# Kernel tuning notes

Measured on AMD Instinct MI355X. Metric: run time of the kernel, lower is better.

## Reference

```python
import jax, jax.numpy as jnp
import numpy as np

N = 50000        # number of nodes
E = 1600000      # number of (directed) edges, ~degree 32
D = 128          # latent_dim
L = 2            # num_layers
NEG_SLOPE = 0.01 # torch F.leaky_relu default


def setup_inputs() -> dict:
    key = jax.random.key(0)
    k1, k2, k3, k4 = jax.random.split(key, 4)
    h = jax.random.normal(k1, (N, D), dtype=jnp.float32)
    src = jax.random.randint(k2, (E,), 0, N, dtype=jnp.int32)
    dst = jax.random.randint(k3, (E,), 0, N, dtype=jnp.int32)
    # attn_fc per layer: Linear(2*D, 1, bias=False) -> weight vector of length 2*D
    att_w = jax.random.normal(k4, (L, 2 * D), dtype=jnp.float32) * 0.1
    return {"h": h, "src": src, "dst": dst, "att_w": att_w}


def _segment_softmax(e, seg, n):
    # numerically-stable softmax over edges grouped by destination node
    m = jax.ops.segment_max(e, seg, num_segments=n)      # [N]
    ex = jnp.exp(e - m[seg])                             # [E]
    s = jax.ops.segment_sum(ex, seg, num_segments=n)     # [N]
    return ex / s[seg]


def reference(h, src, dst, att_w):
    n, d = h.shape
    for l in range(att_w.shape[0]):
        w_src = att_w[l, :d]   # weight applied to edges.src['h']
        w_dst = att_w[l, d:]   # weight applied to edges.dst['h']
        # a = attn_fc(concat(h_src, h_dst)) = h_src @ w_src + h_dst @ w_dst
        a = h[src] @ w_src + h[dst] @ w_dst               # [E]
        e = jnp.where(a > 0, a, NEG_SLOPE * a)            # leaky_relu
        alpha = _segment_softmax(e, dst, n)               # edge_softmax by dst
        # update_all: m = h_src * e ; h_dst = sum(m)
        h = jax.ops.segment_sum(h[src] * alpha[:, None], dst, num_segments=n)
    return h
```

## Files before the change

### kernel.cpp

```cpp
#include <hip/hip_runtime.h>
#include <hip/hip_fp16.h>
#include <math.h>

#define NEG_SLOPE 0.01f
#define BKT_BITS 7
#define BKT_MASK 127
#define SBLOCKS  256
#define STPB     512


__global__ void build_st_kernel(const int* __restrict__ dst, int* __restrict__ blockhist,
                                int E, int NB, int nq, int qchunk,
                                const float* __restrict__ h, const float* __restrict__ att_w_l,
                                float* __restrict__ s, float* __restrict__ t,
                                __half* __restrict__ h16, int N) {
    extern __shared__ int lh[];
    if (blockIdx.x < SBLOCKS) {
        for (int k = threadIdx.x; k < NB; k += blockDim.x) lh[k] = 0;
        __syncthreads();
        int b = blockIdx.x;
        int qbeg = b * qchunk, qend = min(nq, qbeg + qchunk);
        for (int q = qbeg + (int)threadIdx.x; q < qend; q += blockDim.x) {
            int e = q << 2;
            if (e + 3 < E) {
                int4 d4 = *(const int4*)(dst + e);
                atomicAdd(&lh[d4.x >> BKT_BITS], 1);
                atomicAdd(&lh[d4.y >> BKT_BITS], 1);
                atomicAdd(&lh[d4.z >> BKT_BITS], 1);
                atomicAdd(&lh[d4.w >> BKT_BITS], 1);
            } else {
                for (int j = e; j < E; ++j) atomicAdd(&lh[dst[j] >> BKT_BITS], 1);
            }
        }
        __syncthreads();
        for (int k = threadIdx.x; k < NB; k += blockDim.x)
            blockhist[k * SBLOCKS + blockIdx.x] = lh[k];
    } else {
        int sb  = blockIdx.x - SBLOCKS;
        int gid = sb * (int)blockDim.x + threadIdx.x;
        int wid = gid >> 6;
        int lane = threadIdx.x & 63;
        int half = lane >> 5;
        int hl   = lane & 31;
        int v    = wid * 2 + half;
        if (v >= N) return;
        float4 hv = ((const float4*)(h + (size_t)v * 128))[hl];
        __half2 p01 = __floats2half2_rn(hv.x, hv.y);
        __half2 p23 = __floats2half2_rn(hv.z, hv.w);
        float2 packed;
        packed.x = *(const float*)&p01;
        packed.y = *(const float*)&p23;
        ((float2*)(h16 + (size_t)v * 128))[hl] = packed;
        float4 ws = ((const float4*)att_w_l)[hl];
        float4 wd = ((const float4*)(att_w_l + 128))[hl];
        float ps = hv.x * ws.x + hv.y * ws.y + hv.z * ws.z + hv.w * ws.w;
        float pt = hv.x * wd.x + hv.y * wd.y + hv.z * wd.z + hv.w * wd.w;
        for (int off = 16; off > 0; off >>= 1) {
            ps += __shfl_down(ps, off);
            pt += __shfl_down(pt, off);
        }
        if (hl == 0) { s[v] = ps; t[v] = pt; }
    }
}

__global__ void scan1_kernel(const int* __restrict__ in, int* __restrict__ local_excl,
                             int* __restrict__ partials, int n) {
    __shared__ int sm[1024];
    int i = blockIdx.x * 1024 + threadIdx.x;
    int x = (i < n) ? in[i] : 0;
    sm[threadIdx.x] = x;
    __syncthreads();
    for (int off = 1; off < 1024; off <<= 1) {
        int y = (threadIdx.x >= (unsigned)off) ? sm[threadIdx.x - off] : 0;
        __syncthreads();
        sm[threadIdx.x] += y;
        __syncthreads();
    }
    if (i < n) local_excl[i] = sm[threadIdx.x] - x;
    if (threadIdx.x == 1023) partials[blockIdx.x] = sm[1023];
}

__global__ void scan2_kernel(int* __restrict__ partials, int nchunks) {
    __shared__ int sm[1024];
    int x = (threadIdx.x < (unsigned)nchunks) ? partials[threadIdx.x] : 0;
    sm[threadIdx.x] = x;
    __syncthreads();
    for (int off = 1; off < 1024; off <<= 1) {
        int y = (threadIdx.x >= (unsigned)off) ? sm[threadIdx.x - off] : 0;
        __syncthreads();
        sm[threadIdx.x] += y;
        __syncthreads();
    }
    partials[threadIdx.x] = sm[threadIdx.x] - x;
    if (threadIdx.x == 1023) partials[1024] = sm[1023];
}

__device__ __forceinline__ int bh_at(const int* __restrict__ local_ex,
                                     const int* __restrict__ partials, int i) {
    return local_ex[i] + partials[i >> 10];
}

__global__ void bksplit_kernel(const int* __restrict__ src, const int* __restrict__ dst,
                               const int* __restrict__ local_ex, const int* __restrict__ partials,
                               unsigned* __restrict__ pairs,
                               int E, int NB, int nq, int qchunk) {
    extern __shared__ int lm[];
    int* lbase = lm;
    int* lcnt  = lm + NB;
    int b = blockIdx.x;
    for (int k = threadIdx.x; k < NB; k += blockDim.x) {
        lbase[k] = bh_at(local_ex, partials, k * SBLOCKS + b);
        lcnt[k]  = 0;
    }
    __syncthreads();
    int qbeg = b * qchunk, qend = min(nq, qbeg + qchunk);
    for (int q = qbeg + (int)threadIdx.x; q < qend; q += blockDim.x) {
        int e = q << 2;
        if (e + 3 < E) {
            int4 d4 = *(const int4*)(dst + e);
            int4 s4 = *(const int4*)(src + e);
            int k0 = d4.x >> BKT_BITS;
            int p0 = lbase[k0] + atomicAdd(&lcnt[k0], 1);
            pairs[p0] = ((unsigned)s4.x << BKT_BITS) | (unsigned)(d4.x & BKT_MASK);
            int k1 = d4.y >> BKT_BITS;
            int p1 = lbase[k1] + atomicAdd(&lcnt[k1], 1);
            pairs[p1] = ((unsigned)s4.y << BKT_BITS) | (unsigned)(d4.y & BKT_MASK);
            int k2 = d4.z >> BKT_BITS;
            int p2 = lbase[k2] + atomicAdd(&lcnt[k2], 1);
            pairs[p2] = ((unsigned)s4.z << BKT_BITS) | (unsigned)(d4.z & BKT_MASK);
            int k3 = d4.w >> BKT_BITS;
            int p3 = lbase[k3] + atomicAdd(&lcnt[k3], 1);
            pairs[p3] = ((unsigned)s4.w << BKT_BITS) | (unsigned)(d4.w & BKT_MASK);
        } else {
            for (int j = e; j < E; ++j) {
                int d = dst[j];
                int k = d >> BKT_BITS;
                int pos = lbase[k] + atomicAdd(&lcnt[k], 1);
                pairs[pos] = ((unsigned)src[j] << BKT_BITS) | (unsigned)(d & BKT_MASK);
            }
        }
    }
}

__global__ void csr_build_kernel(const unsigned* __restrict__ pairs,
                                 const int* __restrict__ local_ex, const int* __restrict__ partials,
                                 int* __restrict__ row_ptr, int* __restrict__ csr_src,
                                 int E, int N, int NB) {
    __shared__ int ldeg[128];
    __shared__ int lscan[128];
    __shared__ int lpos[128];
    int k = blockIdx.x;
    int bbase = bh_at(local_ex, partials, k * SBLOCKS);
    int bend  = (k == NB - 1) ? E : bh_at(local_ex, partials, (k + 1) * SBLOCKS);
    if (threadIdx.x < 128) ldeg[threadIdx.x] = 0;
    __syncthreads();
    for (int i = bbase + (int)threadIdx.x; i < bend; i += blockDim.x)
        atomicAdd(&ldeg[pairs[i] & BKT_MASK], 1);
    __syncthreads();
    int x = (threadIdx.x < 128) ? ldeg[threadIdx.x] : 0;
    if (threadIdx.x < 128) lscan[threadIdx.x] = x;
    __syncthreads();
    for (int off = 1; off < 128; off <<= 1) {
        int y = 0;
        if (threadIdx.x < 128 && threadIdx.x >= (unsigned)off) y = lscan[threadIdx.x - off];
        __syncthreads();
        if (threadIdx.x < 128) lscan[threadIdx.x] += y;
        __syncthreads();
    }
    if (threadIdx.x < 128) {
        int excl = lscan[threadIdx.x] - x;
        int node = (k << BKT_BITS) + threadIdx.x;
        if (node < N) row_ptr[node] = bbase + excl;
        lpos[threadIdx.x] = excl;
    }
    if (k == NB - 1 && threadIdx.x == 0) row_ptr[N] = E;
    __syncthreads();
    for (int i = bbase + (int)threadIdx.x; i < bend; i += blockDim.x) {
        unsigned p = pairs[i];
        int pos = atomicAdd(&lpos[p & BKT_MASK], 1);
        csr_src[bbase + pos] = (int)(p >> BKT_BITS);
    }
}


__device__ __forceinline__ void gath8(const __half* __restrict__ hin, int u, float w,
                                      int qlane, float acc[8]) {
    float4 r = ((const float4*)(hin + ((size_t)(unsigned)u << 7)))[qlane];
    const __half2* hp = (const __half2*)&r;
    #pragma unroll
    for (int d = 0; d < 4; ++d) {
        acc[2 * d]     = fmaf(__low2float(hp[d]),  w, acc[2 * d]);
        acc[2 * d + 1] = fmaf(__high2float(hp[d]), w, acc[2 * d + 1]);
    }
}

template<bool LAST>
__global__ __launch_bounds__(256, 8)
void agg_kernel(const __half* __restrict__ hin, const float* __restrict__ s,
                const float* __restrict__ t, const int* __restrict__ row_ptr,
                const int* __restrict__ csr_src,
                __half* __restrict__ hout16, float* __restrict__ outf,
                const float* __restrict__ att_w_next,
                float* __restrict__ s2, float* __restrict__ t2, int n) {
    int gid   = blockIdx.x * blockDim.x + threadIdx.x;
    int v     = gid >> 6;
    int lane  = threadIdx.x & 63;
    if (v >= n) return;
    int quad  = lane >> 4;
    int qlane = lane & 15;

    int beg = row_ptr[v];
    int end = row_ptr[v + 1];
    float tv = t[v];

    float acc[8] = {0.f, 0.f, 0.f, 0.f, 0.f, 0.f, 0.f, 0.f};
    float lsum_l = 0.f;

    for (int base = beg; base < end; base += 64) {
        int cnt = end - base;
        if (cnt > 64) cnt = 64;
        int idx = base + min(lane, cnt - 1);
        int u   = csr_src[idx];
        float a = s[u] + tv;
        float e = (a > 0.f) ? a : NEG_SLOPE * a;
        float wl = (lane < cnt) ? __expf(e) : 0.f;
        lsum_l += wl;
        int steps = (cnt + 3) >> 2;
        int k = 0;
        for (; k + 3 < steps; k += 4) {
            int sl0 = (k << 2) + quad;
            int   u0 = __shfl(u, sl0);       float w0 = __shfl(wl, sl0);
            int   u1 = __shfl(u, sl0 + 4);   float w1 = __shfl(wl, sl0 + 4);
            int   u2 = __shfl(u, sl0 + 8);   float w2 = __shfl(wl, sl0 + 8);
            int   u3 = __shfl(u, sl0 + 12);  float w3 = __shfl(wl, sl0 + 12);
            gath8(hin, u0, w0, qlane, acc);
            gath8(hin, u1, w1, qlane, acc);
            gath8(hin, u2, w2, qlane, acc);
            gath8(hin, u3, w3, qlane, acc);
        }
        for (; k < steps; ++k) {
            int sl = (k << 2) + quad;
            int   u0 = __shfl(u, sl);
            float w0 = __shfl(wl, sl);
            gath8(hin, u0, w0, qlane, acc);
        }
    }
    #pragma unroll
    for (int j = 0; j < 8; ++j) {
        acc[j] += __shfl_xor(acc[j], 16);
        acc[j] += __shfl_xor(acc[j], 32);
    }
    float lsum = lsum_l;
    for (int off = 32; off > 0; off >>= 1) lsum += __shfl_xor(lsum, off);
    float inv_l = (lsum > 0.f) ? (1.0f / lsum) : 0.f;
    #pragma unroll
    for (int j = 0; j < 8; ++j) acc[j] *= inv_l;

    if (LAST) {
        if (quad == 0) {
            float4* op = (float4*)(outf + (size_t)v * 128);
            op[2 * qlane]     = make_float4(acc[0], acc[1], acc[2], acc[3]);
            op[2 * qlane + 1] = make_float4(acc[4], acc[5], acc[6], acc[7]);
        }
    } else {
        if (quad == 0) {
            __half2 p0 = __floats2half2_rn(acc[0], acc[1]);
            __half2 p1 = __floats2half2_rn(acc[2], acc[3]);
            __half2 p2 = __floats2half2_rn(acc[4], acc[5]);
            __half2 p3 = __floats2half2_rn(acc[6], acc[7]);
            int4 pk;
            pk.x = *(const int*)&p0; pk.y = *(const int*)&p1;
            pk.z = *(const int*)&p2; pk.w = *(const int*)&p3;
            ((int4*)(hout16 + (size_t)v * 128))[qlane] = pk;
        }
        float4 ws0 = ((const float4*)att_w_next)[2 * qlane];
        float4 ws1 = ((const float4*)att_w_next)[2 * qlane + 1];
        float4 wd0 = ((const float4*)(att_w_next + 128))[2 * qlane];
        float4 wd1 = ((const float4*)(att_w_next + 128))[2 * qlane + 1];
        float ps = acc[0] * ws0.x + acc[1] * ws0.y + acc[2] * ws0.z + acc[3] * ws0.w
                 + acc[4] * ws1.x + acc[5] * ws1.y + acc[6] * ws1.z + acc[7] * ws1.w;
        float pt = acc[0] * wd0.x + acc[1] * wd0.y + acc[2] * wd0.z + acc[3] * wd0.w
                 + acc[4] * wd1.x + acc[5] * wd1.y + acc[6] * wd1.z + acc[7] * wd1.w;
        for (int off = 8; off > 0; off >>= 1) {
            ps += __shfl_down(ps, off);
            pt += __shfl_down(pt, off);
        }
        if (lane == 0) { s2[v] = ps; t2[v] = pt; }
    }
}


extern "C" void kernel_launch(void* const* d_in, const int* in_sizes, int n_in,
                              void* d_out, int out_size, void* d_ws, size_t ws_size,
                              hipStream_t stream) {
    const float* h0    = (const float*)d_in[0];
    const int*   src   = (const int*)d_in[1];
    const int*   dst   = (const int*)d_in[2];
    const float* att_w = (const float*)d_in[3];
    int N = in_sizes[0] / 128;
    int E = in_sizes[1];
    int L = in_sizes[3] / 256;
    float* out = (float*)d_out;

    int NB = (N + BKT_MASK) >> BKT_BITS;
    int n2 = NB * SBLOCKS;
    int nq = (E + 3) >> 2;
    int qchunk = (nq + SBLOCKS - 1) / SBLOCKS;
    int nch2 = (n2 + 1023) / 1024;

    char* ws = (char*)d_ws;
    size_t off = 0;
    auto alloc = [&](size_t bytes) -> void* {
        void* p = ws + off;
        off = (off + bytes + 511) & ~(size_t)511;
        return p;
    };
    int*      row_ptr   = (int*)     alloc((size_t)(N + 1) * 4);
    int*      csr_src   = (int*)     alloc((size_t)E * 4);
    float*    s1        = (float*)   alloc((size_t)N * 4);
    float*    t1        = (float*)   alloc((size_t)N * 4);
    float*    s2        = (float*)   alloc((size_t)N * 4);
    float*    t2        = (float*)   alloc((size_t)N * 4);
    __half*   hA        = (__half*)  alloc((size_t)N * 128 * 2);
    __half*   hB        = (__half*)  alloc((size_t)N * 128 * 2);
    unsigned* pairs     = (unsigned*)alloc((size_t)E * 4);
    int*      blockhist = (int*)     alloc((size_t)n2 * 4);
    int*      local_ex  = (int*)     alloc((size_t)n2 * 4);
    int*      partials  = (int*)     alloc(1025 * 4);

    int st_blocks = ((N + 1) / 2 + 7) / 8;
    build_st_kernel<<<SBLOCKS + st_blocks, STPB, NB * 4, stream>>>(
        dst, blockhist, E, NB, nq, qchunk, h0, att_w, s1, t1, hA, N);
    scan1_kernel<<<nch2, 1024, 0, stream>>>(blockhist, local_ex, partials, n2);
    scan2_kernel<<<1, 1024, 0, stream>>>(partials, nch2);
    bksplit_kernel<<<SBLOCKS, STPB, 2 * NB * 4, stream>>>(src, dst, local_ex, partials,
                                                          pairs, E, NB, nq, qchunk);
    csr_build_kernel<<<NB, 512, 0, stream>>>(pairs, local_ex, partials,
                                             row_ptr, csr_src, E, N, NB);

    const int tb = 256;
    int node_blocks = (N * 64 + tb - 1) / tb;

    __half* hin = hA;
    __half* hnx = hB;
    float *sc = s1, *tc = t1, *sn = s2, *tn = t2;
    for (int l = 0; l < L; ++l) {
        if (l == L - 1) {
            agg_kernel<true><<<node_blocks, tb, 0, stream>>>(
                hin, sc, tc, row_ptr, csr_src, nullptr, out, nullptr, nullptr, nullptr, N);
        } else {
            agg_kernel<false><<<node_blocks, tb, 0, stream>>>(
                hin, sc, tc, row_ptr, csr_src, hnx, nullptr,
                att_w + (size_t)(l + 1) * 256, sn, tn, N);
            __half* tmp = hin; hin = hnx; hnx = tmp;
            float* tf;
            tf = sc; sc = sn; sn = tf;
            tf = tc; tc = tn; tn = tf;
        }
    }
}
```

Before: 214.9 us.

## Fuse CSR build pipeline into one cooperative kernel with grid syncs

```diff
diff --git a/kernel.cpp b/kernel.cpp
--- a/kernel.cpp
+++ b/kernel.cpp
@@ -1,184 +1,161 @@
 #include <hip/hip_runtime.h>
 #include <hip/hip_fp16.h>
+#include <hip/hip_cooperative_groups.h>
 #include <math.h>
+
+namespace cg = cooperative_groups;
 
 #define NEG_SLOPE 0.01f
 #define BKT_BITS 7
 #define BKT_MASK 127
 #define SBLOCKS  256
 #define STPB     512
-
-
-__global__ void build_st_kernel(const int* __restrict__ dst, int* __restrict__ blockhist,
-                                int E, int NB, int nq, int qchunk,
-                                const float* __restrict__ h, const float* __restrict__ att_w_l,
-                                float* __restrict__ s, float* __restrict__ t,
-                                __half* __restrict__ h16, int N) {
-    extern __shared__ int lh[];
-    if (blockIdx.x < SBLOCKS) {
-        for (int k = threadIdx.x; k < NB; k += blockDim.x) lh[k] = 0;
-        __syncthreads();
-        int b = blockIdx.x;
-        int qbeg = b * qchunk, qend = min(nq, qbeg + qchunk);
-        for (int q = qbeg + (int)threadIdx.x; q < qend; q += blockDim.x) {
+#define MAXNB    512
+
+__global__ void build_coop_kernel(const int* __restrict__ src, const int* __restrict__ dst,
+                                  const float* __restrict__ h, const float* __restrict__ att_w_l,
+                                  int* __restrict__ g_total, unsigned* __restrict__ pairs,
+                                  int* __restrict__ row_ptr, int* __restrict__ csr_src,
+                                  float* __restrict__ s, float* __restrict__ t,
+                                  __half* __restrict__ h16,
+                                  int E, int N, int NB, int nq, int qchunk) {
+    __shared__ int lh[MAXNB];
+    __shared__ int lbb[MAXNB];
+    __shared__ int sc[STPB];
+    __shared__ int lstart[MAXNB + 1];
+    __shared__ int ldeg[128];
+    __shared__ int lscan[128];
+    __shared__ int lpos[128];
+
+    cg::grid_group grid = cg::this_grid();
+    int b   = blockIdx.x;
+    int tid = threadIdx.x;
+
+    for (int k = tid; k < NB; k += blockDim.x) lh[k] = 0;
+    __syncthreads();
+    int qbeg = b * qchunk, qend = min(nq, qbeg + qchunk);
+    for (int q = qbeg + tid; q < qend; q += blockDim.x) {
+        int e = q << 2;
+        if (e + 3 < E) {
+            int4 d4 = *(const int4*)(dst + e);
+            atomicAdd(&lh[d4.x >> BKT_BITS], 1);
+            atomicAdd(&lh[d4.y >> BKT_BITS], 1);
+            atomicAdd(&lh[d4.z >> BKT_BITS], 1);
+            atomicAdd(&lh[d4.w >> BKT_BITS], 1);
+        } else {
+            for (int j = e; j < E; ++j) atomicAdd(&lh[dst[j] >> BKT_BITS], 1);
+        }
+    }
+    __syncthreads();
+    for (int k = tid; k < NB; k += blockDim.x)
+        lbb[k] = atomicAdd(&g_total[k], lh[k]);
+
+    {
+        int lane = tid & 63;
+        int halfw = lane >> 5;
+        int hl = lane & 31;
+        int wv = b * (blockDim.x >> 6) + (tid >> 6);
+        int vstride = gridDim.x * (blockDim.x >> 6) * 2;
+        for (int v = wv * 2 + halfw; v < N; v += vstride) {
+            float4 hv = ((const float4*)(h + (size_t)v * 128))[hl];
+            __half2 p01 = __floats2half2_rn(hv.x, hv.y);
+            __half2 p23 = __floats2half2_rn(hv.z, hv.w);
+            float2 packed;
+            packed.x = *(const float*)&p01;
+            packed.y = *(const float*)&p23;
+            ((float2*)(h16 + (size_t)v * 128))[hl] = packed;
+            float4 ws = ((const float4*)att_w_l)[hl];
+            float4 wd = ((const float4*)(att_w_l + 128))[hl];
+            float ps = hv.x * ws.x + hv.y * ws.y + hv.z * ws.z + hv.w * ws.w;
+            float pt = hv.x * wd.x + hv.y * wd.y + hv.z * wd.z + hv.w * wd.w;
+            for (int off = 16; off > 0; off >>= 1) {
+                ps += __shfl_down(ps, off);
+                pt += __shfl_down(pt, off);
+            }
+            if (hl == 0) { s[v] = ps; t[v] = pt; }
+        }
+    }
+    grid.sync();
+
+    {
+        int x = (tid < NB) ? g_total[tid] : 0;
+        sc[tid] = x;
+        __syncthreads();
+        for (int off = 1; off < STPB; off <<= 1) {
+            int y = (tid >= (unsigned)off) ? sc[tid - off] : 0;
+            __syncthreads();
+            sc[tid] += y;
+            __syncthreads();
+        }
+        if (tid < NB) lstart[tid] = sc[tid] - x;
+        if (tid == 0) lstart[NB] = E;
+        __syncthreads();
+        for (int k = tid; k < NB; k += blockDim.x) {
+            lbb[k] += lstart[k];
+            lh[k] = 0;
+        }
+        __syncthreads();
+        for (int q = qbeg + tid; q < qend; q += blockDim.x) {
             int e = q << 2;
             if (e + 3 < E) {
                 int4 d4 = *(const int4*)(dst + e);
-                atomicAdd(&lh[d4.x >> BKT_BITS], 1);
-                atomicAdd(&lh[d4.y >> BKT_BITS], 1);
-                atomicAdd(&lh[d4.z >> BKT_BITS], 1);
-                atomicAdd(&lh[d4.w >> BKT_BITS], 1);
+                int4 s4 = *(const int4*)(src + e);
+                int k0 = d4.x >> BKT_BITS;
+                int p0 = lbb[k0] + atomicAdd(&lh[k0], 1);
+                pairs[p0] = ((unsigned)s4.x << BKT_BITS) | (unsigned)(d4.x & BKT_MASK);
+                int k1 = d4.y >> BKT_BITS;
+                int p1 = lbb[k1] + atomicAdd(&lh[k1], 1);
+                pairs[p1] = ((unsigned)s4.y << BKT_BITS) | (unsigned)(d4.y & BKT_MASK);
+                int k2 = d4.z >> BKT_BITS;
+                int p2 = lbb[k2] + atomicAdd(&lh[k2], 1);
+                pairs[p2] = ((unsigned)s4.z << BKT_BITS) | (unsigned)(d4.z & BKT_MASK);
+                int k3 = d4.w >> BKT_BITS;
+                int p3 = lbb[k3] + atomicAdd(&lh[k3], 1);
+                pairs[p3] = ((unsigned)s4.w << BKT_BITS) | (unsigned)(d4.w & BKT_MASK);
             } else {
-                for (int j = e; j < E; ++j) atomicAdd(&lh[dst[j] >> BKT_BITS], 1);
+                for (int j = e; j < E; ++j) {
+                    int d = dst[j];
+                    int k = d >> BKT_BITS;
+                    int pos = lbb[k] + atomicAdd(&lh[k], 1);
+                    pairs[pos] = ((unsigned)src[j] << BKT_BITS) | (unsigned)(d & BKT_MASK);
+                }
             }
         }
-        __syncthreads();
-        for (int k = threadIdx.x; k < NB; k += blockDim.x)
-            blockhist[k * SBLOCKS + blockIdx.x] = lh[k];
-    } else {
-        int sb  = blockIdx.x - SBLOCKS;
-        int gid = sb * (int)blockDim.x + threadIdx.x;
-        int wid = gid >> 6;
-        int lane = threadIdx.x & 63;
-        int half = lane >> 5;
-        int hl   = lane & 31;
-        int v    = wid * 2 + half;
-        if (v >= N) return;
-        float4 hv = ((const float4*)(h + (size_t)v * 128))[hl];
-        __half2 p01 = __floats2half2_rn(hv.x, hv.y);
-        __half2 p23 = __floats2half2_rn(hv.z, hv.w);
-        float2 packed;
-        packed.x = *(const float*)&p01;
-        packed.y = *(const float*)&p23;
-        ((float2*)(h16 + (size_t)v * 128))[hl] = packed;
-        float4 ws = ((const float4*)att_w_l)[hl];
-        float4 wd = ((const float4*)(att_w_l + 128))[hl];
-        float ps = hv.x * ws.x + hv.y * ws.y + hv.z * ws.z + hv.w * ws.w;
-        float pt = hv.x * wd.x + hv.y * wd.y + hv.z * wd.z + hv.w * wd.w;
-        for (int off = 16; off > 0; off >>= 1) {
-            ps += __shfl_down(ps, off);
-            pt += __shfl_down(pt, off);
-        }
-        if (hl == 0) { s[v] = ps; t[v] = pt; }
-    }
-}
-
-__global__ void scan1_kernel(const int* __restrict__ in, int* __restrict__ local_excl,
-                             int* __restrict__ partials, int n) {
-    __shared__ int sm[1024];
-    int i = blockIdx.x * 1024 + threadIdx.x;
-    int x = (i < n) ? in[i] : 0;
-    sm[threadIdx.x] = x;
-    __syncthreads();
-    for (int off = 1; off < 1024; off <<= 1) {
-        int y = (threadIdx.x >= (unsigned)off) ? sm[threadIdx.x - off] : 0;
-        __syncthreads();
-        sm[threadIdx.x] += y;
-        __syncthreads();
-    }
-    if (i < n) local_excl[i] = sm[threadIdx.x] - x;
-    if (threadIdx.x == 1023) partials[blockIdx.x] = sm[1023];
-}
-
-__global__ void scan2_kernel(int* __restrict__ partials, int nchunks) {
-    __shared__ int sm[1024];
-    int x = (threadIdx.x < (unsigned)nchunks) ? partials[threadIdx.x] : 0;
-    sm[threadIdx.x] = x;
-    __syncthreads();
-    for (int off = 1; off < 1024; off <<= 1) {
-        int y = (threadIdx.x >= (unsigned)off) ? sm[threadIdx.x - off] : 0;
-        __syncthreads();
-        sm[threadIdx.x] += y;
-        __syncthreads();
-    }
-    partials[threadIdx.x] = sm[threadIdx.x] - x;
-    if (threadIdx.x == 1023) partials[1024] = sm[1023];
-}
-
-__device__ __forceinline__ int bh_at(const int* __restrict__ local_ex,
-                                     const int* __restrict__ partials, int i) {
-    return local_ex[i] + partials[i >> 10];
-}
-
-__global__ void bksplit_kernel(const int* __restrict__ src, const int* __restrict__ dst,
-                               const int* __restrict__ local_ex, const int* __restrict__ partials,
-                               unsigned* __restrict__ pairs,
-                               int E, int NB, int nq, int qchunk) {
-    extern __shared__ int lm[];
-    int* lbase = lm;
-    int* lcnt  = lm + NB;
-    int b = blockIdx.x;
-    for (int k = threadIdx.x; k < NB; k += blockDim.x) {
-        lbase[k] = bh_at(local_ex, partials, k * SBLOCKS + b);
-        lcnt[k]  = 0;
-    }
-    __syncthreads();
-    int qbeg = b * qchunk, qend = min(nq, qbeg + qchunk);
-    for (int q = qbeg + (int)threadIdx.x; q < qend; q += blockDim.x) {
-        int e = q << 2;
-        if (e + 3 < E) {
-            int4 d4 = *(const int4*)(dst + e);
-            int4 s4 = *(const int4*)(src + e);
-            int k0 = d4.x >> BKT_BITS;
-            int p0 = lbase[k0] + atomicAdd(&lcnt[k0], 1);
-            pairs[p0] = ((unsigned)s4.x << BKT_BITS) | (unsigned)(d4.x & BKT_MASK);
-            int k1 = d4.y >> BKT_BITS;
-            int p1 = lbase[k1] + atomicAdd(&lcnt[k1], 1);
-            pairs[p1] = ((unsigned)s4.y << BKT_BITS) | (unsigned)(d4.y & BKT_MASK);
-            int k2 = d4.z >> BKT_BITS;
-            int p2 = lbase[k2] + atomicAdd(&lcnt[k2], 1);
-            pairs[p2] = ((unsigned)s4.z << BKT_BITS) | (unsigned)(d4.z & BKT_MASK);
-            int k3 = d4.w >> BKT_BITS;
-            int p3 = lbase[k3] + atomicAdd(&lcnt[k3], 1);
-            pairs[p3] = ((unsigned)s4.w << BKT_BITS) | (unsigned)(d4.w & BKT_MASK);
-        } else {
-            for (int j = e; j < E; ++j) {
-                int d = dst[j];
-                int k = d >> BKT_BITS;
-                int pos = lbase[k] + atomicAdd(&lcnt[k], 1);
-                pairs[pos] = ((unsigned)src[j] << BKT_BITS) | (unsigned)(d & BKT_MASK);
-            }
-        }
-    }
-}
-
-__global__ void csr_build_kernel(const unsigned* __restrict__ pairs,
-                                 const int* __restrict__ local_ex, const int* __restrict__ partials,
-                                 int* __restrict__ row_ptr, int* __restrict__ csr_src,
-                                 int E, int N, int NB) {
-    __shared__ int ldeg[128];
-    __shared__ int lscan[128];
-    __shared__ int lpos[128];
-    int k = blockIdx.x;
-    int bbase = bh_at(local_ex, partials, k * SBLOCKS);
-    int bend  = (k == NB - 1) ? E : bh_at(local_ex, partials, (k + 1) * SBLOCKS);
-    if (threadIdx.x < 128) ldeg[threadIdx.x] = 0;
-    __syncthreads();
-    for (int i = bbase + (int)threadIdx.x; i < bend; i += blockDim.x)
-        atomicAdd(&ldeg[pairs[i] & BKT_MASK], 1);
-    __syncthreads();
-    int x = (threadIdx.x < 128) ? ldeg[threadIdx.x] : 0;
-    if (threadIdx.x < 128) lscan[threadIdx.x] = x;
-    __syncthreads();
-    for (int off = 1; off < 128; off <<= 1) {
-        int y = 0;
-        if (threadIdx.x < 128 && threadIdx.x >= (unsigned)off) y = lscan[threadIdx.x - off];
-        __syncthreads();
-        if (threadIdx.x < 128) lscan[threadIdx.x] += y;
-        __syncthreads();
-    }
-    if (threadIdx.x < 128) {
-        int excl = lscan[threadIdx.x] - x;
-        int node = (k << BKT_BITS) + threadIdx.x;
-        if (node < N) row_ptr[node] = bbase + excl;
-        lpos[threadIdx.x] = excl;
-    }
-    if (k == NB - 1 && threadIdx.x == 0) row_ptr[N] = E;
-    __syncthreads();
-    for (int i = bbase + (int)threadIdx.x; i < bend; i += blockDim.x) {
-        unsigned p = pairs[i];
-        int pos = atomicAdd(&lpos[p & BKT_MASK], 1);
-        csr_src[bbase + pos] = (int)(p >> BKT_BITS);
+    }
+    grid.sync();
+
+    if (b == 0 && tid == 0) row_ptr[N] = E;
+    for (int kb = b; kb < NB; kb += gridDim.x) {
+        int bbase = lstart[kb];
+        int bend  = lstart[kb + 1];
+        if (tid < 128) ldeg[tid] = 0;
+        __syncthreads();
+        for (int i = bbase + tid; i < bend; i += blockDim.x)
+            atomicAdd(&ldeg[pairs[i] & BKT_MASK], 1);
+        __syncthreads();
+        int x = (tid < 128) ? ldeg[tid] : 0;
+        if (tid < 128) lscan[tid] = x;
+        __syncthreads();
+        for (int off = 1; off < 128; off <<= 1) {
+            int y = 0;
+            if (tid < 128 && tid >= (unsigned)off) y = lscan[tid - off];
+            __syncthreads();
+            if (tid < 128) lscan[tid] += y;
+            __syncthreads();
+        }
+        if (tid < 128) {
+            int excl = lscan[tid] - x;
+            int node = (kb << BKT_BITS) + tid;
+            if (node < N) row_ptr[node] = bbase + excl;
+            lpos[tid] = excl;
+        }
+        __syncthreads();
+        for (int i = bbase + tid; i < bend; i += blockDim.x) {
+            unsigned p = pairs[i];
+            int pos = atomicAdd(&lpos[p & BKT_MASK], 1);
+            csr_src[bbase + pos] = (int)(p >> BKT_BITS);
+        }
+        __syncthreads();
     }
 }
 
@@ -303,10 +280,8 @@
     float* out = (float*)d_out;
 
     int NB = (N + BKT_MASK) >> BKT_BITS;
-    int n2 = NB * SBLOCKS;
     int nq = (E + 3) >> 2;
     int qchunk = (nq + SBLOCKS - 1) / SBLOCKS;
-    int nch2 = (n2 + 1023) / 1024;
 
     char* ws = (char*)d_ws;
     size_t off = 0;
@@ -324,19 +299,18 @@
     __half*   hA        = (__half*)  alloc((size_t)N * 128 * 2);
     __half*   hB        = (__half*)  alloc((size_t)N * 128 * 2);
     unsigned* pairs     = (unsigned*)alloc((size_t)E * 4);
-    int*      blockhist = (int*)     alloc((size_t)n2 * 4);
-    int*      local_ex  = (int*)     alloc((size_t)n2 * 4);
-    int*      partials  = (int*)     alloc(1025 * 4);
-
-    int st_blocks = ((N + 1) / 2 + 7) / 8;
-    build_st_kernel<<<SBLOCKS + st_blocks, STPB, NB * 4, stream>>>(
-        dst, blockhist, E, NB, nq, qchunk, h0, att_w, s1, t1, hA, N);
-    scan1_kernel<<<nch2, 1024, 0, stream>>>(blockhist, local_ex, partials, n2);
-    scan2_kernel<<<1, 1024, 0, stream>>>(partials, nch2);
-    bksplit_kernel<<<SBLOCKS, STPB, 2 * NB * 4, stream>>>(src, dst, local_ex, partials,
-                                                          pairs, E, NB, nq, qchunk);
-    csr_build_kernel<<<NB, 512, 0, stream>>>(pairs, local_ex, partials,
-                                             row_ptr, csr_src, E, N, NB);
+    int*      g_total   = (int*)     alloc((size_t)(NB + 1) * 4);
+
+    hipMemsetAsync(g_total, 0, (size_t)NB * 4, stream);
+
+    void* cargs[] = {
+        (void*)&src, (void*)&dst, (void*)&h0, (void*)&att_w,
+        (void*)&g_total, (void*)&pairs, (void*)&row_ptr, (void*)&csr_src,
+        (void*)&s1, (void*)&t1, (void*)&hA,
+        (void*)&E, (void*)&N, (void*)&NB, (void*)&nq, (void*)&qchunk
+    };
+    hipLaunchCooperativeKernel(reinterpret_cast<void*>(build_coop_kernel),
+                               dim3(SBLOCKS), dim3(STPB), cargs, 0, stream);
 
     const int tb = 256;
     int node_blocks = (N * 64 + tb - 1) / tb;
```

Result: slower. 303.5 us (+41.2%).

## Replace two-pass global scan with atomic bucket offsets and per-block scan

Applied to the files above, without the earlier changes.

```diff
diff --git a/kernel.cpp b/kernel.cpp
--- a/kernel.cpp
+++ b/kernel.cpp
@@ -7,9 +7,11 @@
 #define BKT_MASK 127
 #define SBLOCKS  256
 #define STPB     512
-
-
-__global__ void build_st_kernel(const int* __restrict__ dst, int* __restrict__ blockhist,
+#define MAXNB    512
+
+
+__global__ void build_st_kernel(const int* __restrict__ dst, int* __restrict__ g_total,
+                                int* __restrict__ g_lbb,
                                 int E, int NB, int nq, int qchunk,
                                 const float* __restrict__ h, const float* __restrict__ att_w_l,
                                 float* __restrict__ s, float* __restrict__ t,
@@ -34,7 +36,7 @@
         }
         __syncthreads();
         for (int k = threadIdx.x; k < NB; k += blockDim.x)
-            blockhist[k * SBLOCKS + blockIdx.x] = lh[k];
+            g_lbb[k * SBLOCKS + b] = atomicAdd(&g_total[k], lh[k]);
     } else {
         int sb  = blockIdx.x - SBLOCKS;
         int gid = sb * (int)blockDim.x + threadIdx.x;
@@ -63,58 +65,40 @@
     }
 }
 
-__global__ void scan1_kernel(const int* __restrict__ in, int* __restrict__ local_excl,
-                             int* __restrict__ partials, int n) {
-    __shared__ int sm[1024];
-    int i = blockIdx.x * 1024 + threadIdx.x;
-    int x = (i < n) ? in[i] : 0;
-    sm[threadIdx.x] = x;
-    __syncthreads();
-    for (int off = 1; off < 1024; off <<= 1) {
-        int y = (threadIdx.x >= (unsigned)off) ? sm[threadIdx.x - off] : 0;
-        __syncthreads();
-        sm[threadIdx.x] += y;
-        __syncthreads();
-    }
-    if (i < n) local_excl[i] = sm[threadIdx.x] - x;
-    if (threadIdx.x == 1023) partials[blockIdx.x] = sm[1023];
-}
-
-__global__ void scan2_kernel(int* __restrict__ partials, int nchunks) {
-    __shared__ int sm[1024];
-    int x = (threadIdx.x < (unsigned)nchunks) ? partials[threadIdx.x] : 0;
-    sm[threadIdx.x] = x;
-    __syncthreads();
-    for (int off = 1; off < 1024; off <<= 1) {
-        int y = (threadIdx.x >= (unsigned)off) ? sm[threadIdx.x - off] : 0;
-        __syncthreads();
-        sm[threadIdx.x] += y;
-        __syncthreads();
-    }
-    partials[threadIdx.x] = sm[threadIdx.x] - x;
-    if (threadIdx.x == 1023) partials[1024] = sm[1023];
-}
-
-__device__ __forceinline__ int bh_at(const int* __restrict__ local_ex,
-                                     const int* __restrict__ partials, int i) {
-    return local_ex[i] + partials[i >> 10];
-}
-
 __global__ void bksplit_kernel(const int* __restrict__ src, const int* __restrict__ dst,
-                               const int* __restrict__ local_ex, const int* __restrict__ partials,
-                               unsigned* __restrict__ pairs,
+                               const int* __restrict__ g_total, const int* __restrict__ g_lbb,
+                               int* __restrict__ g_lstart, unsigned* __restrict__ pairs,
                                int E, int NB, int nq, int qchunk) {
-    extern __shared__ int lm[];
-    int* lbase = lm;
-    int* lcnt  = lm + NB;
-    int b = blockIdx.x;
-    for (int k = threadIdx.x; k < NB; k += blockDim.x) {
-        lbase[k] = bh_at(local_ex, partials, k * SBLOCKS + b);
+    __shared__ int sc[STPB];
+    __shared__ int lstart[MAXNB + 1];
+    __shared__ int lbase[MAXNB];
+    __shared__ int lcnt[MAXNB];
+    int b   = blockIdx.x;
+    int tid = threadIdx.x;
+
+    int x = (tid < NB) ? g_total[tid] : 0;
+    sc[tid] = x;
+    __syncthreads();
+    for (int off = 1; off < STPB; off <<= 1) {
+        int y = (tid >= (unsigned)off) ? sc[tid - off] : 0;
+        __syncthreads();
+        sc[tid] += y;
+        __syncthreads();
+    }
+    if (tid < NB) lstart[tid] = sc[tid] - x;
+    if (tid == 0) lstart[NB] = E;
+    __syncthreads();
+    for (int k = tid; k < NB; k += blockDim.x) {
+        lbase[k] = lstart[k] + g_lbb[k * SBLOCKS + b];
         lcnt[k]  = 0;
     }
-    __syncthreads();
+    if (b == 0) {
+        for (int k = tid; k <= NB; k += blockDim.x) g_lstart[k] = lstart[k];
+    }
+    __syncthreads();
+
     int qbeg = b * qchunk, qend = min(nq, qbeg + qchunk);
-    for (int q = qbeg + (int)threadIdx.x; q < qend; q += blockDim.x) {
+    for (int q = qbeg + tid; q < qend; q += blockDim.x) {
         int e = q << 2;
         if (e + 3 < E) {
             int4 d4 = *(const int4*)(dst + e);
@@ -143,15 +127,15 @@
 }
 
 __global__ void csr_build_kernel(const unsigned* __restrict__ pairs,
-                                 const int* __restrict__ local_ex, const int* __restrict__ partials,
+                                 const int* __restrict__ g_lstart,
                                  int* __restrict__ row_ptr, int* __restrict__ csr_src,
                                  int E, int N, int NB) {
     __shared__ int ldeg[128];
     __shared__ int lscan[128];
     __shared__ int lpos[128];
     int k = blockIdx.x;
-    int bbase = bh_at(local_ex, partials, k * SBLOCKS);
-    int bend  = (k == NB - 1) ? E : bh_at(local_ex, partials, (k + 1) * SBLOCKS);
+    int bbase = g_lstart[k];
+    int bend  = g_lstart[k + 1];
     if (threadIdx.x < 128) ldeg[threadIdx.x] = 0;
     __syncthreads();
     for (int i = bbase + (int)threadIdx.x; i < bend; i += blockDim.x)
@@ -303,10 +287,8 @@
     float* out = (float*)d_out;
 
     int NB = (N + BKT_MASK) >> BKT_BITS;
-    int n2 = NB * SBLOCKS;
     int nq = (E + 3) >> 2;
     int qchunk = (nq + SBLOCKS - 1) / SBLOCKS;
-    int nch2 = (n2 + 1023) / 1024;
 
     char* ws = (char*)d_ws;
     size_t off = 0;
@@ -324,19 +306,18 @@
     __half*   hA        = (__half*)  alloc((size_t)N * 128 * 2);
     __half*   hB        = (__half*)  alloc((size_t)N * 128 * 2);
     unsigned* pairs     = (unsigned*)alloc((size_t)E * 4);
-    int*      blockhist = (int*)     alloc((size_t)n2 * 4);
-    int*      local_ex  = (int*)     alloc((size_t)n2 * 4);
-    int*      partials  = (int*)     alloc(1025 * 4);
+    int*      g_lbb     = (int*)     alloc((size_t)NB * SBLOCKS * 4);
+    int*      g_total   = (int*)     alloc((size_t)(NB + 1) * 4);
+    int*      g_lstart  = (int*)     alloc((size_t)(NB + 1) * 4);
+
+    hipMemsetAsync(g_total, 0, (size_t)NB * 4, stream);
 
     int st_blocks = ((N + 1) / 2 + 7) / 8;
     build_st_kernel<<<SBLOCKS + st_blocks, STPB, NB * 4, stream>>>(
-        dst, blockhist, E, NB, nq, qchunk, h0, att_w, s1, t1, hA, N);
-    scan1_kernel<<<nch2, 1024, 0, stream>>>(blockhist, local_ex, partials, n2);
-    scan2_kernel<<<1, 1024, 0, stream>>>(partials, nch2);
-    bksplit_kernel<<<SBLOCKS, STPB, 2 * NB * 4, stream>>>(src, dst, local_ex, partials,
-                                                          pairs, E, NB, nq, qchunk);
-    csr_build_kernel<<<NB, 512, 0, stream>>>(pairs, local_ex, partials,
-                                             row_ptr, csr_src, E, N, NB);
+        dst, g_total, g_lbb, E, NB, nq, qchunk, h0, att_w, s1, t1, hA, N);
+    bksplit_kernel<<<SBLOCKS, STPB, 0, stream>>>(src, dst, g_total, g_lbb, g_lstart,
+                                                 pairs, E, NB, nq, qchunk);
+    csr_build_kernel<<<NB, 512, 0, stream>>>(pairs, g_lstart, row_ptr, csr_src, E, N, NB);
 
     const int tb = 256;
     int node_blocks = (N * 64 + tb - 1) / tb;
```

Result: slower. 220.3 us (+2.5%).
